# Kernel optimization log

Hardware: AMD Instinct MI355X
Metric: run time of the kernel (lower is better)

The kernel has to match this reference:

```python
import jax, jax.numpy as jnp
import numpy as np

B, K, V = 8192, 1024, 2


def setup_inputs() -> dict:
    key = jax.random.key(0)
    k1, k2, k3, k4, k5, k6 = jax.random.split(key, 6)
    z = jax.random.normal(k1, (B, K), dtype=jnp.float32)
    # -1 means no intervention for that sample
    intervention_target = jax.random.randint(k2, (B,), -1, K)
    intervention_variant = jax.random.randint(k3, (B,), 0, V)
    raw_adjacency = jax.random.normal(k4, (K, K), dtype=jnp.float32) * 0.05
    intervention_means = jax.random.normal(k5, (K, V), dtype=jnp.float32)
    intervention_log_scales = jax.random.normal(k6, (K, V), dtype=jnp.float32) * 0.1
    return {
        "z": z,
        "intervention_target": intervention_target,
        "intervention_variant": intervention_variant,
        "raw_adjacency": raw_adjacency,
        "intervention_means": intervention_means,
        "intervention_log_scales": intervention_log_scales,
    }


def _scm_forward(z, target, variant, raw_adjacency, means, log_scales):
    Kd = z.shape[1]
    # strictly-lower-triangular adjacency (row j holds parents of node j)
    A = raw_adjacency * jnp.tril(jnp.ones((Kd, Kd), z.dtype), k=-1)

    def step(u, xs):
        a_row, mean_row, logsc_row, z_j, j = xs
        # forward substitution: u_j = z_j + sum_{i<j} A[j,i] * u_i
        # columns >= j of u are still zero and A row is zero there too
        value = z_j + u @ a_row  # [B]
        # intervention overwrite for samples with target == j
        m = mean_row[variant]                 # [B]
        s = jnp.exp(logsc_row[variant])       # [B]
        value = jnp.where(target == j, m + s * z_j, value)
        u = jax.lax.dynamic_update_slice(u, value[:, None], (0, j))
        return u, None

    u0 = jnp.zeros_like(z)
    xs = (A, means, log_scales, z.T, jnp.arange(Kd))
    u, _ = jax.lax.scan(step, u0, xs)
    return u


def reference(z, intervention_target, intervention_variant, raw_adjacency,
              intervention_means, intervention_log_scales):
    return _scm_forward(z, intervention_target, intervention_variant,
                        raw_adjacency, intervention_means, intervention_log_scales)
```

## Files before the change

### kernel.cpp

```cpp
#include <hip/hip_runtime.h>
#include <hip/hip_bf16.h>
#include <cstdint>

#define KDIM 1024
#define BDIM 8192
#define VDIM 2
#define NBLK 16

#if defined(__has_builtin)
#if __has_builtin(__builtin_amdgcn_global_load_lds)
#define HAS_GLL 1
#endif
#endif
#ifndef HAS_GLL
#define HAS_GLL 0
#endif

typedef __attribute__((ext_vector_type(8))) short short8;
typedef __attribute__((ext_vector_type(4))) float f32x4;

__device__ inline unsigned short f2bf(float x) {
  unsigned u = __builtin_bit_cast(unsigned, x);
  u = (u + 0x7FFFu + ((u >> 16) & 1u)) >> 16;
  return (unsigned short)u;
}

__device__ inline float bf2f(unsigned short x) {
  return __builtin_bit_cast(float, (unsigned)x << 16);
}

__device__ inline void qtile_map(int t, int& bi, int& bj) {
  if (t < 64) {
    bi = t >> 3;
    bj = 8 + (t & 7);
  } else {
    int r = t - 64;
    const int c = r >> 4;
    r &= 15;
    bi = 8 * c + (r >> 2);
    bj = 8 * c + 4 + (r & 3);
  }
}


#define STAGE_T(DST, SRC, ROW0, COL0, LD)                                   \
  {                                                                         \
    const float* _s = (SRC);                                                \
    _Pragma("unroll") for (int _p = 0; _p < 4; ++_p) {                      \
      const int _m = _p * 16 + rw;                                          \
      float4 _v = *(const float4*)(_s + (size_t)((ROW0) + _m) * (LD) +      \
                                   (COL0) + 4 * k4);                        \
      (DST)[4 * k4 + 0][_m] = _v.x;                                         \
      (DST)[4 * k4 + 1][_m] = _v.y;                                         \
      (DST)[4 * k4 + 2][_m] = _v.z;                                         \
      (DST)[4 * k4 + 3][_m] = _v.w;                                         \
    }                                                                       \
  }

#define STAGE_D(DST, SRC, ROW0, COL0, LD)                                   \
  {                                                                         \
    const float* _s = (SRC);                                                \
    _Pragma("unroll") for (int _p = 0; _p < 4; ++_p) {                      \
      const int _kk = _p * 16 + rw;                                         \
      *(float4*)&(DST)[_kk][4 * k4] =                                       \
          *(const float4*)(_s + (size_t)((ROW0) + _kk) * (LD) + (COL0) +    \
                           4 * k4);                                         \
    }                                                                       \
  }

#define ZERO_ACC                                                            \
  _Pragma("unroll") for (int _a = 0; _a < 4; ++_a)                          \
      _Pragma("unroll") for (int _b = 0; _b < 4; ++_b) acc[_a][_b] = 0.f;

__device__ __forceinline__ void mac64(const float (*Ls)[68],
                                      const float (*Rs)[68], int tm, int tn,
                                      float acc[4][4]) {
#pragma unroll 4
  for (int k = 0; k < 64; ++k) {
    const float4 av = *(const float4*)&Ls[k][4 * tm];
    const float4 bv = *(const float4*)&Rs[k][4 * tn];
    const float aa[4] = {av.x, av.y, av.z, av.w};
    const float bb4[4] = {bv.x, bv.y, bv.z, bv.w};
#pragma unroll
    for (int a = 0; a < 4; ++a)
#pragma unroll
      for (int b = 0; b < 4; ++b) acc[a][b] += aa[a] * bb4[b];
  }
}

#define STORE_MT(R0, C0)                                                    \
  _Pragma("unroll") for (int _a = 0; _a < 4; ++_a) {                        \
    *(float4*)(MT + (size_t)((R0) + 4 * tm + _a) * KDIM + (C0) + 4 * tn) =  \
        make_float4(acc[_a][0], acc[_a][1], acc[_a][2], acc[_a][3]);        \
  }

#define MBF_TILE(R0, C0, BUF)                                               \
  {                                                                         \
    __syncthreads();                                                        \
    _Pragma("unroll") for (int _a = 0; _a < 4; ++_a)                        \
        _Pragma("unroll") for (int _b = 0; _b < 4; ++_b)                    \
            (BUF)[4 * tm + _a][4 * tn + _b] = acc[_a][_b];                  \
    __syncthreads();                                                        \
    const int _tr = tid >> 4, _tc = tid & 15;                               \
    _Pragma("unroll") for (int _p = 0; _p < 4; ++_p) {                      \
      const int _il = _p * 16 + _tr;                                        \
      ushort4 _o;                                                           \
      _o.x = f2bf((BUF)[4 * _tc + 0][_il]);                                 \
      _o.y = f2bf((BUF)[4 * _tc + 1][_il]);                                 \
      _o.z = f2bf((BUF)[4 * _tc + 2][_il]);                                 \
      _o.w = f2bf((BUF)[4 * _tc + 3][_il]);                                 \
      *(ushort4*)(Mbf + (size_t)((C0) + _il) * KDIM + (R0) + 4 * _tc) = _o; \
    }                                                                       \
  }

__global__ __launch_bounds__(256) void comb01(const float* __restrict__ A,
                                              float* __restrict__ MT,
                                              unsigned short* __restrict__ Mbf,
                                              const float* __restrict__ Z,
                                              unsigned short* __restrict__ Zbf,
                                              float* __restrict__ Pscr,
                                              int do_zbf) {
  if (blockIdx.x >= NBLK) {
    const int wid = blockIdx.x - NBLK;
    const int nw = gridDim.x - NBLK;
    const int idx0 = wid * 256 + threadIdx.x;
    const int stride = nw * 256;
    const float4 z4 = make_float4(0.f, 0.f, 0.f, 0.f);
    const uint4 u4 = make_uint4(0u, 0u, 0u, 0u);

    for (int i = idx0; i < 256 * 1024; i += stride) {
      const int blk = i >> 10, off = i & 1023;
      const int bi = blk >> 4, bj = blk & 15;
      if (bi <= bj) continue;
      *(float4*)(MT + (size_t)(bi * 64 + (off >> 4)) * KDIM + bj * 64 +
                 4 * (off & 15)) = z4;
    }
    for (int i = idx0; i < 96 * 1024; i += stride) {
      const int t = i >> 10, off = i & 1023;
      int bi, bj;
      qtile_map(t, bi, bj);
      *(float4*)(MT + (size_t)(bi * 64 + (off >> 4)) * KDIM + bj * 64 +
                 4 * (off & 15)) = z4;
    }
    for (int i = idx0; i < 98304; i += stride)
      *(float4*)(Pscr + 4 * (size_t)i) = z4;
    for (int i = idx0; i < 256 * 512; i += stride) {
      const int blk = i >> 9, off = i & 511;
      const int bi = blk >> 4, bj = blk & 15;
      if (bi >= bj) continue;
      *(uint4*)(Mbf + (size_t)(bi * 64 + (off >> 3)) * KDIM + bj * 64 +
                8 * (off & 7)) = u4;
    }
    if (do_zbf) {
      for (int i = idx0; i < BDIM * KDIM / 4; i += stride) {
        float4 v = *(const float4*)(Z + 4 * (size_t)i);
        ushort4 o;
        o.x = f2bf(v.x);
        o.y = f2bf(v.y);
        o.z = f2bf(v.z);
        o.w = f2bf(v.w);
        *(ushort4*)(Zbf + 4 * (size_t)i) = o;
      }
    }
    return;
  }

  int b = blockIdx.x;
  const int rt = b & 1;
  const int jt = (b >> 1) & 1;
  const int s = b >> 2;
  const int base = s * 256;

  __shared__ float shpool[6 * 64 * 68];
  float (*Ls)[68] = (float(*)[68])(shpool);
  float (*Rs)[68] = (float(*)[68])(shpool + 4352);
  float (*tQ0L)[68] = (float(*)[68])(shpool + 2 * 4352);
  float (*tQ0H)[68] = (float(*)[68])(shpool + 3 * 4352);
  float (*tP0)[68] = (float(*)[68])(shpool + 4 * 4352);
  float (*tP1)[68] = (float(*)[68])(shpool + 5 * 4352);

  const int tid = threadIdx.x;
  const int k4 = tid & 15;
  const int rw = tid >> 4;
  const int tm = tid >> 4;
  const int tn = tid & 15;
  float acc[4][4];

  {
    float* Tt = shpool;
    float* As4 = shpool + 2 * 4352;
    const int g = tid >> 6;
    const int l = tid & 63;
    const int dbase = base + g * 64;
    float* Asg = As4 + g * 4160;

    for (int r = 0; r < 64; ++r)
      Asg[r * 65 + l] = A[(size_t)(dbase + r) * KDIM + dbase + l];
    __syncthreads();

    {
      const int h = l >> 5, c = l & 31;
      const float* Ah = Asg + (32 * h) * 65 + 32 * h;
      float m[32];
#pragma unroll
      for (int r = 0; r < 32; ++r) m[r] = (r == c) ? 1.f : 0.f;
#pragma unroll
      for (int r = 1; r < 32; ++r) {
        float a0 = 0.f, a1 = 0.f;
#pragma unroll
        for (int i = 0; i < 32; ++i) {
          if (i >= r) break;
          if (i & 1) a1 += Ah[r * 65 + i] * m[i];
          else       a0 += Ah[r * 65 + i] * m[i];
        }
        const float v = a0 + a1;
        m[r] = (r > c) ? v : m[r];
      }
      float* Th = Tt + g * 2112 + h * 1056;
#pragma unroll
      for (int r = 0; r < 32; ++r) Th[r * 33 + c] = m[r];
    }
    __syncthreads();

    const int tm8 = l >> 3, tn8 = l & 7;
    {
      float u[4][4];
#pragma unroll
      for (int a = 0; a < 4; ++a)
#pragma unroll
        for (int b2 = 0; b2 < 4; ++b2) u[a][b2] = 0.f;
      const float* T1 = Tt + g * 2112;
#pragma unroll
      for (int ki = 0; ki < 8; ++ki) {
        float4 av[4], bv[4];
#pragma unroll
        for (int a = 0; a < 4; ++a)
          av[a] = *(const float4*)&Asg[(32 + 4 * tm8 + a) * 65 + 4 * ki];
#pragma unroll
        for (int j = 0; j < 4; ++j)
          bv[j] = *(const float4*)&T1[(4 * ki + j) * 33 + 4 * tn8];
#pragma unroll
        for (int a = 0; a < 4; ++a) {
          const float aa[4] = {av[a].x, av[a].y, av[a].z, av[a].w};
#pragma unroll
          for (int j = 0; j < 4; ++j) {
            const float bb[4] = {bv[j].x, bv[j].y, bv[j].z, bv[j].w};
#pragma unroll
            for (int b2 = 0; b2 < 4; ++b2) u[a][b2] += aa[j] * bb[b2];
          }
        }
      }
#pragma unroll
      for (int a = 0; a < 4; ++a)
#pragma unroll
        for (int b2 = 0; b2 < 4; ++b2)
          Asg[(4 * tm8 + a) * 32 + 4 * tn8 + b2] = u[a][b2];
    }
    __syncthreads();

    {
      float t21[4][4];
#pragma unroll
      for (int a = 0; a < 4; ++a)
#pragma unroll
        for (int b2 = 0; b2 < 4; ++b2) t21[a][b2] = 0.f;
      const float* T2 = Tt + g * 2112 + 1056;
#pragma unroll
      for (int ki = 0; ki < 8; ++ki) {
        float4 av[4], bv[4];
#pragma unroll
        for (int a = 0; a < 4; ++a)
          av[a] = *(const float4*)&T2[(4 * tm8 + a) * 33 + 4 * ki];
#pragma unroll
        for (int j = 0; j < 4; ++j)
          bv[j] = *(const float4*)&Asg[(4 * ki + j) * 32 + 4 * tn8];
#pragma unroll
        for (int a = 0; a < 4; ++a) {
          const float aa[4] = {av[a].x, av[a].y, av[a].z, av[a].w};
#pragma unroll
          for (int j = 0; j < 4; ++j) {
            const float bb[4] = {bv[j].x, bv[j].y, bv[j].z, bv[j].w};
#pragma unroll
            for (int b2 = 0; b2 < 4; ++b2) t21[a][b2] += aa[j] * bb[b2];
          }
        }
      }
#pragma unroll
      for (int a = 0; a < 4; ++a)
#pragma unroll
        for (int b2 = 0; b2 < 4; ++b2)
          Asg[1024 + (4 * tm8 + a) * 32 + 4 * tn8 + b2] = t21[a][b2];
    }
    __syncthreads();

    {
      const float* T21 = Asg + 1024;
      const float* Tg = Tt + g * 2112;
      for (int r4 = 0; r4 < 16; ++r4) {
        float vals[4];
#pragma unroll
        for (int j = 0; j < 4; ++j) {
          const int r = 4 * r4 + j;
          float v;
          if (r < 32)
            v = (l < 32) ? Tg[r * 33 + l] : 0.f;
          else
            v = (l < 32) ? T21[(r - 32) * 32 + l]
                         : Tg[1056 + (r - 32) * 33 + (l - 32)];
          vals[j] = v;
        }
        *(float4*)(MT + (size_t)(dbase + l) * KDIM + dbase + 4 * r4) =
            make_float4(vals[0], vals[1], vals[2], vals[3]);
      }
      if (jt == 0 && rt == 0) {
        for (int r = 0; r < 64; ++r) {
          float v;
          if (r < 32)
            v = (l < 32) ? Tg[r * 33 + l] : 0.f;
          else
            v = (l < 32) ? T21[(r - 32) * 32 + l]
                         : Tg[1056 + (r - 32) * 33 + (l - 32)];
          Mbf[(size_t)(dbase + r) * KDIM + dbase + l] = f2bf(v);
        }
      }
    }
    __syncthreads();
  }

  if (jt == 0) {
    STAGE_T(Ls, MT, base, base, KDIM);
    STAGE_T(Rs, A, base + 64, base, KDIM);
    __syncthreads();
    ZERO_ACC;
    mac64(Ls, Rs, tm, tn, acc);
    __syncthreads();
#pragma unroll
    for (int a = 0; a < 4; ++a)
#pragma unroll
      for (int b2 = 0; b2 < 4; ++b2) tP0[4 * tn + b2][4 * tm + a] = acc[a][b2];
    STAGE_D(Rs, MT, base + 64, base + 64, KDIM);
    __syncthreads();
    ZERO_ACC;
    mac64(tP0, Rs, tm, tn, acc);
    __syncthreads();
#pragma unroll
    for (int a = 0; a < 4; ++a)
#pragma unroll
      for (int b2 = 0; b2 < 4; ++b2) tQ0L[4 * tn + b2][4 * tm + a] = acc[a][b2];
    if (rt == 0) {
      STORE_MT(base, base + 64);
      MBF_TILE(base, base + 64, Rs);
    }
  }
  __syncthreads();

  if (rt == 1) {
    STAGE_T(Ls, MT, base + 128, base + 128, KDIM);
    STAGE_T(Rs, A, base + 192, base + 128, KDIM);
    __syncthreads();
    ZERO_ACC;
    mac64(Ls, Rs, tm, tn, acc);
    __syncthreads();
#pragma unroll
    for (int a = 0; a < 4; ++a)
#pragma unroll
      for (int b2 = 0; b2 < 4; ++b2) tP1[4 * tn + b2][4 * tm + a] = acc[a][b2];
    STAGE_D(Rs, MT, base + 192, base + 192, KDIM);
    __syncthreads();
    ZERO_ACC;
    mac64(tP1, Rs, tm, tn, acc);
    __syncthreads();
#pragma unroll
    for (int a = 0; a < 4; ++a)
#pragma unroll
      for (int b2 = 0; b2 < 4; ++b2) tQ0H[4 * tm + a][4 * tn + b2] = acc[a][b2];
    if (jt == 1) {
      STORE_MT(base + 128, base + 192);
      MBF_TILE(base + 128, base + 192, Rs);
    }
  }
  __syncthreads();

  STAGE_T(Ls, MT, base + 64 * jt, base + 64 * jt, KDIM);
  __syncthreads();
  for (int kb2 = 0; kb2 <= rt; ++kb2) {
    ZERO_ACC;
    for (int kb = jt; kb < 2; ++kb) {
      STAGE_T(Rs, A, base + 128 + 64 * kb2, base + 64 * kb, KDIM);
      __syncthreads();
      mac64(kb == jt ? Ls : tQ0L, Rs, tm, tn, acc);
      __syncthreads();
    }
    if (kb2 == 0) {
#pragma unroll
      for (int a = 0; a < 4; ++a)
#pragma unroll
        for (int b2 = 0; b2 < 4; ++b2) tP0[4 * tn + b2][4 * tm + a] = acc[a][b2];
    } else {
#pragma unroll
      for (int a = 0; a < 4; ++a)
#pragma unroll
        for (int b2 = 0; b2 < 4; ++b2) tP1[4 * tn + b2][4 * tm + a] = acc[a][b2];
    }
  }
  __syncthreads();

  ZERO_ACC;
  if (rt == 0) {
    STAGE_D(Rs, MT, base + 128, base + 128, KDIM);
    __syncthreads();
    mac64(tP0, Rs, tm, tn, acc);
    __syncthreads();
  } else {
    mac64(tP0, tQ0H, tm, tn, acc);
    __syncthreads();
    STAGE_D(Rs, MT, base + 192, base + 192, KDIM);
    __syncthreads();
    mac64(tP1, Rs, tm, tn, acc);
    __syncthreads();
  }
  STORE_MT(base + 64 * jt, base + 128 + 64 * rt);
  MBF_TILE(base + 64 * jt, base + 128 + 64 * rt, Rs);
}

template <int T>
__global__ __launch_bounds__(256) void comb_p(const float* __restrict__ A,
                                              const float* __restrict__ MT,
                                              float* __restrict__ Pt) {
  int b = blockIdx.x;
  const int kc = b % T; b /= T;
  const int rt = b % T; b /= T;
  const int jt = b % T; b /= T;
  const int c = b;
  if (kc < jt) return;
  const int h = 64 * T;
  const int base = c * 2 * h;

  __shared__ float Ls[64][68];
  __shared__ float Rs[64][68];
  const int tid = threadIdx.x;
  const int k4 = tid & 15;
  const int rw = tid >> 4;
  const int tm = tid >> 4;
  const int tn = tid & 15;
  float acc[4][4];
  ZERO_ACC;

  STAGE_T(Ls, MT, base + 64 * jt, base + 64 * kc, KDIM);
  STAGE_T(Rs, A, base + h + 64 * rt, base + 64 * kc, KDIM);
  __syncthreads();
  mac64(Ls, Rs, tm, tn, acc);

  float* P0 = Pt + (size_t)c * h * h;
#pragma unroll
  for (int a = 0; a < 4; ++a)
#pragma unroll
    for (int b2 = 0; b2 < 4; ++b2)
      unsafeAtomicAdd(P0 + (size_t)(64 * jt + 4 * tm + a) * h + 64 * rt +
                          4 * tn + b2,
                      acc[a][b2]);
}

template <int T>
__global__ __launch_bounds__(256) void comb_q(float* __restrict__ MT,
                                              const float* __restrict__ Pt) {
  int b = blockIdx.x;
  const int kc = b % T; b /= T;
  const int rt = b % T; b /= T;
  const int jt = b % T; b /= T;
  const int c = b;
  if (kc > rt) return;
  const int h = 64 * T;
  const int base = c * 2 * h;

  __shared__ float Ls[64][68];
  __shared__ float Rs[64][68];
  const int tid = threadIdx.x;
  const int k4 = tid & 15;
  const int rw = tid >> 4;
  const int tm = tid >> 4;
  const int tn = tid & 15;
  float acc[4][4];
  ZERO_ACC;

  const float* P0 = Pt + (size_t)c * h * h;
  STAGE_T(Ls, P0, 64 * jt, 64 * kc, h);
  STAGE_D(Rs, MT, base + h + 64 * kc, base + h + 64 * rt, KDIM);
  __syncthreads();
  mac64(Ls, Rs, tm, tn, acc);

#pragma unroll
  for (int a = 0; a < 4; ++a)
#pragma unroll
    for (int b2 = 0; b2 < 4; ++b2)
      unsafeAtomicAdd(MT + (size_t)(base + 64 * jt + 4 * tm + a) * KDIM +
                          base + h + 64 * rt + 4 * tn + b2,
                      acc[a][b2]);
}

__global__ __launch_bounds__(256) void mt2bf96(const float* __restrict__ MT,
                                               unsigned short* __restrict__ Mbf) {
  int bi, bj;
  qtile_map(blockIdx.x, bi, bj);
  const int j0 = bi * 64;
  const int i0 = bj * 64;
  __shared__ float tile[64][65];

  const int tr = threadIdx.x >> 4;
  const int tc = threadIdx.x & 15;
#pragma unroll
  for (int p = 0; p < 4; ++p) {
    const int rj = p * 16 + tr;
    float4 v = *(const float4*)(MT + (size_t)(j0 + rj) * KDIM + i0 + 4 * tc);
    tile[rj][4 * tc + 0] = v.x;
    tile[rj][4 * tc + 1] = v.y;
    tile[rj][4 * tc + 2] = v.z;
    tile[rj][4 * tc + 3] = v.w;
  }
  __syncthreads();
#pragma unroll
  for (int p = 0; p < 4; ++p) {
    const int il = p * 16 + tr;
    ushort4 o;
    o.x = f2bf(tile[4 * tc + 0][il]);
    o.y = f2bf(tile[4 * tc + 1][il]);
    o.z = f2bf(tile[4 * tc + 2][il]);
    o.w = f2bf(tile[4 * tc + 3][il]);
    *(ushort4*)(Mbf + (size_t)(i0 + il) * KDIM + j0 + 4 * tc) = o;
  }
}

#define LDB 72

template <int ZBF>
__global__ __launch_bounds__(256) void gemm_mfma(
    const float* __restrict__ Z, const unsigned short* __restrict__ Zbf,
    const unsigned short* __restrict__ Mbf, const float* __restrict__ MT,
    const int* __restrict__ tgt, const int* __restrict__ var,
    const float* __restrict__ means, const float* __restrict__ lsc,
    float* __restrict__ C) {
  __shared__ unsigned short As[128][LDB];
#if HAS_GLL
  __shared__ unsigned short Bs[128][64];
#else
  __shared__ unsigned short Bs[128][LDB];
#endif
  __shared__ float scoef[128];
  __shared__ int stb[128];

  const int d = blockIdx.x;
  const int xbl = d & 7;
  const int nir = (d >> 3) & 7;
  const int xbh = d >> 6;
  const int xb = xbh * 8 + xbl;
  const int ni = (xb & 32) ? (7 - nir) : nir;
  const int b0 = xb * 128;
  const int i0 = ni * 128;

  const int tid = threadIdx.x;
  const int w = tid >> 6;
  const int lane = tid & 63;
  const int wr = w >> 1, wc = w & 1;
  const int mlane = lane & 15;
  const int q = lane >> 4;

  const int rq = tid >> 4, kq = tid & 15;
  const int cb = tid >> 3, ck = tid & 7;

  f32x4 acc[4][4];
#pragma unroll
  for (int a = 0; a < 4; ++a)
#pragma unroll
    for (int b = 0; b < 4; ++b) acc[a][b] = (f32x4){0.f, 0.f, 0.f, 0.f};

  const int nkb = 2 * (ni + 1);
  for (int kb = 0; kb < nkb; ++kb) {
    const int k0 = kb * 64;
    if (ZBF) {
#pragma unroll
      for (int p = 0; p < 4; ++p) {
        const int r = p * 32 + cb;
        *(uint4*)&As[r][8 * ck] =
            *(const uint4*)(Zbf + (size_t)(b0 + r) * KDIM + k0 + 8 * ck);
      }
    } else {
#pragma unroll
      for (int p = 0; p < 8; ++p) {
        const int r = p * 16 + rq;
        float4 zv = *(const float4*)(Z + (size_t)(b0 + r) * KDIM + k0 + 4 * kq);
        ushort4 o;
        o.x = f2bf(zv.x);
        o.y = f2bf(zv.y);
        o.z = f2bf(zv.z);
        o.w = f2bf(zv.w);
        *(ushort4*)&As[r][4 * kq] = o;
      }
    }
#if HAS_GLL
    {
      const int rl = lane >> 3;
      const int ch = lane & 7;
#pragma unroll
      for (int i = 0; i < 4; ++i) {
        const int row = w * 32 + i * 8 + rl;
        const int sch = ch ^ (row & 7);
        const unsigned short* src =
            Mbf + (size_t)(i0 + row) * KDIM + k0 + sch * 8;
        __builtin_amdgcn_global_load_lds(
            (const __attribute__((address_space(1))) void*)src,
            (__attribute__((address_space(3))) void*)&Bs[w * 32 + i * 8][0],
            16, 0, 0);
      }
    }
#else
#pragma unroll
    for (int p = 0; p < 4; ++p) {
      const int c = p * 32 + cb;
      *(uint4*)&Bs[c][8 * ck] =
          *(const uint4*)(Mbf + (size_t)(i0 + c) * KDIM + k0 + 8 * ck);
    }
#endif
    __syncthreads();
#pragma unroll
    for (int ks = 0; ks < 2; ++ks) {
      const int kf = ks * 32 + q * 8;
      short8 av[4], bv[4];
#pragma unroll
      for (int a = 0; a < 4; ++a)
        av[a] = *(const short8*)&As[wr * 64 + 16 * a + mlane][kf];
#if HAS_GLL
      const char* BsB = (const char*)&Bs[0][0];
#pragma unroll
      for (int b = 0; b < 4; ++b) {
        const int row = wc * 64 + 16 * b + mlane;
        bv[b] = *(const short8*)(BsB + row * 128 +
                                 ((2 * kf) ^ ((row & 7) << 4)));
      }
#else
#pragma unroll
      for (int b = 0; b < 4; ++b)
        bv[b] = *(const short8*)&Bs[wc * 64 + 16 * b + mlane][kf];
#endif
#pragma unroll
      for (int a = 0; a < 4; ++a)
#pragma unroll
        for (int b = 0; b < 4; ++b)
          acc[a][b] =
              __builtin_amdgcn_mfma_f32_16x16x32_bf16(av[a], bv[b], acc[a][b], 0, 0, 0);
    }
    __syncthreads();
  }

  {
    const int s = tid >> 1, h2 = tid & 1;
    const int br = b0 + s;
    const int tb = tgt[br];
    float part = 0.f;
    if (tb >= 0) {
      const int nk16 = (tb >> 4) + 1;
      if (ZBF) {
        const unsigned short* zr = Zbf + (size_t)br * KDIM;
        const unsigned short* mr = Mbf + (size_t)tb * KDIM;
        for (int c16 = h2; c16 < nk16; c16 += 2) {
          const uint4 za = *(const uint4*)(zr + c16 * 16);
          const uint4 zb2 = *(const uint4*)(zr + c16 * 16 + 8);
          const uint4 ma = *(const uint4*)(mr + c16 * 16);
          const uint4 mb2 = *(const uint4*)(mr + c16 * 16 + 8);
          const unsigned zw[8] = {za.x, za.y, za.z, za.w,
                                  zb2.x, zb2.y, zb2.z, zb2.w};
          const unsigned mw[8] = {ma.x, ma.y, ma.z, ma.w,
                                  mb2.x, mb2.y, mb2.z, mb2.w};
#pragma unroll
          for (int wv = 0; wv < 8; ++wv) {
            part += __builtin_bit_cast(float, zw[wv] << 16) *
                    __builtin_bit_cast(float, mw[wv] << 16);
            part += __builtin_bit_cast(float, zw[wv] & 0xFFFF0000u) *
                    __builtin_bit_cast(float, mw[wv] & 0xFFFF0000u);
          }
        }
      } else {
        const float* zr = Z + (size_t)br * KDIM;
        const unsigned short* mr = Mbf + (size_t)tb * KDIM;
        const int nk8 = (tb >> 3) + 1;
        for (int c8 = h2; c8 < nk8; c8 += 2) {
          const float4 z0 = *(const float4*)(zr + c8 * 8);
          const float4 z1 = *(const float4*)(zr + c8 * 8 + 4);
          const ushort4 m0 = *(const ushort4*)(mr + c8 * 8);
          const ushort4 m1 = *(const ushort4*)(mr + c8 * 8 + 4);
          part += z0.x * bf2f(m0.x) + z0.y * bf2f(m0.y) + z0.z * bf2f(m0.z) +
                  z0.w * bf2f(m0.w) + z1.x * bf2f(m1.x) + z1.y * bf2f(m1.y) +
                  z1.z * bf2f(m1.z) + z1.w * bf2f(m1.w);
        }
      }
    }
    part += __shfl_down(part, 1);
    if (h2 == 0) {
      float cf = 0.f;
      int tbs = 0;
      if (tb >= 0) {
        const int v = var[br];
        const float mval = means[tb * VDIM + v];
        const float sval = expf(lsc[tb * VDIM + v]);
        const float zv = Z[(size_t)br * KDIM + tb];
        cf = (mval + sval * zv) - part;
        tbs = tb;
      }
      scoef[s] = cf;
      stb[s] = tbs;
    }
  }
  __syncthreads();

#pragma unroll
  for (int a = 0; a < 4; ++a) {
    const int l0 = wr * 64 + 16 * a + q * 4;
    const int row0 = b0 + l0;
#pragma unroll
    for (int b = 0; b < 4; ++b) {
      const int col = i0 + wc * 64 + 16 * b + mlane;
      float* Cp = C + (size_t)row0 * KDIM + col;
#pragma unroll
      for (int j = 0; j < 4; ++j) {
        const float cf = scoef[l0 + j];
        const float corr = cf * MT[(size_t)stb[l0 + j] * KDIM + col];
        Cp[j * KDIM] = acc[a][b][j] + corr;
      }
    }
  }
}

extern "C" void kernel_launch(void* const* d_in, const int* in_sizes, int n_in,
                              void* d_out, int out_size, void* d_ws,
                              size_t ws_size, hipStream_t stream) {
  const float* z = (const float*)d_in[0];
  const int* tgt = (const int*)d_in[1];
  const int* var = (const int*)d_in[2];
  const float* A = (const float*)d_in[3];
  const float* means = (const float*)d_in[4];
  const float* lsc = (const float*)d_in[5];
  float* out = (float*)d_out;

  char* ws = (char*)d_ws;
  float* MT = (float*)ws;
  unsigned short* Mbf = (unsigned short*)(ws + (4u << 20));
  float* Pt2 = (float*)(ws + (6u << 20));
  float* Pt3 = (float*)(ws + (6u << 20) + (512u << 10));
  unsigned short* Zbf = (unsigned short*)(ws + (7u << 20) + (512u << 10));
  const int use_zbf =
      ws_size >= (7u << 20) + (512u << 10) + (size_t)BDIM * KDIM * 2 ? 1 : 0;

  hipLaunchKernelGGL(comb01, dim3(256), dim3(256), 0, stream, A, MT, Mbf, z,
                     Zbf, Pt2, use_zbf);
  hipLaunchKernelGGL((comb_p<4>), dim3(128), dim3(256), 0, stream, A, MT, Pt2);
  hipLaunchKernelGGL((comb_q<4>), dim3(128), dim3(256), 0, stream, MT, Pt2);
  hipLaunchKernelGGL((comb_p<8>), dim3(512), dim3(256), 0, stream, A, MT, Pt3);
  hipLaunchKernelGGL((comb_q<8>), dim3(512), dim3(256), 0, stream, MT, Pt3);
  hipLaunchKernelGGL(mt2bf96, dim3(96), dim3(256), 0, stream, MT, Mbf);
  if (use_zbf)
    hipLaunchKernelGGL((gemm_mfma<1>), dim3((BDIM / 128) * (KDIM / 128)),
                       dim3(256), 0, stream, z, Zbf, Mbf, MT, tgt, var, means,
                       lsc, out);
  else
    hipLaunchKernelGGL((gemm_mfma<0>), dim3((BDIM / 128) * (KDIM / 128)),
                       dim3(256), 0, stream, z, Zbf, Mbf, MT, tgt, var, means,
                       lsc, out);
}
```

Baseline: 228.7 us.

## Split the fused 256-wide inverse stage into a 128-wide stage plus extra combine level

The first kernel used to invert 256x256 diagonal blocks with 16 blocks doing multi-step combines. It now inverts only 128x128 blocks, using 8 blocks in which only half the threads do the 64x64 triangular inverses. A new comb_p<2>/comb_q<2> launch pair then combines those into 256-wide blocks, and the zeroing and bf16 conversion ranges grow to cover the extra off-diagonal tiles. This shortens the serial chain inside the first kernel, at the cost of two more launches, idle threads in that kernel, and atomic-add based combining.

```diff
diff --git a/kernel.cpp b/kernel.cpp
--- a/kernel.cpp
+++ b/kernel.cpp
@@ -33,12 +33,18 @@
   if (t < 64) {
     bi = t >> 3;
     bj = 8 + (t & 7);
-  } else {
+  } else if (t < 96) {
     int r = t - 64;
     const int c = r >> 4;
     r &= 15;
     bi = 8 * c + (r >> 2);
     bj = 8 * c + 4 + (r & 3);
+  } else {
+    int r = t - 96;
+    const int c = r >> 2;
+    r &= 3;
+    bi = 4 * c + (r >> 1);
+    bj = 4 * c + 2 + (r & 1);
   }
 }
 
@@ -113,16 +119,16 @@
     }                                                                       \
   }
 
-__global__ __launch_bounds__(256) void comb01(const float* __restrict__ A,
+__global__ __launch_bounds__(256) void comb0a(const float* __restrict__ A,
                                               float* __restrict__ MT,
                                               unsigned short* __restrict__ Mbf,
                                               const float* __restrict__ Z,
                                               unsigned short* __restrict__ Zbf,
                                               float* __restrict__ Pscr,
                                               int do_zbf) {
-  if (blockIdx.x >= NBLK) {
-    const int wid = blockIdx.x - NBLK;
-    const int nw = gridDim.x - NBLK;
+  if (blockIdx.x >= 8) {
+    const int wid = blockIdx.x - 8;
+    const int nw = gridDim.x - 8;
     const int idx0 = wid * 256 + threadIdx.x;
     const int stride = nw * 256;
     const float4 z4 = make_float4(0.f, 0.f, 0.f, 0.f);
@@ -135,14 +141,14 @@
       *(float4*)(MT + (size_t)(bi * 64 + (off >> 4)) * KDIM + bj * 64 +
                  4 * (off & 15)) = z4;
     }
-    for (int i = idx0; i < 96 * 1024; i += stride) {
+    for (int i = idx0; i < 112 * 1024; i += stride) {
       const int t = i >> 10, off = i & 1023;
       int bi, bj;
       qtile_map(t, bi, bj);
       *(float4*)(MT + (size_t)(bi * 64 + (off >> 4)) * KDIM + bj * 64 +
                  4 * (off & 15)) = z4;
     }
-    for (int i = idx0; i < 98304; i += stride)
+    for (int i = idx0; i < 114688; i += stride)
       *(float4*)(Pscr + 4 * (size_t)i) = z4;
     for (int i = idx0; i < 256 * 512; i += stride) {
       const int blk = i >> 9, off = i & 511;
@@ -165,19 +171,13 @@
     return;
   }
 
-  int b = blockIdx.x;
-  const int rt = b & 1;
-  const int jt = (b >> 1) & 1;
-  const int s = b >> 2;
-  const int base = s * 256;
-
-  __shared__ float shpool[6 * 64 * 68];
-  float (*Ls)[68] = (float(*)[68])(shpool);
-  float (*Rs)[68] = (float(*)[68])(shpool + 4352);
-  float (*tQ0L)[68] = (float(*)[68])(shpool + 2 * 4352);
-  float (*tQ0H)[68] = (float(*)[68])(shpool + 3 * 4352);
-  float (*tP0)[68] = (float(*)[68])(shpool + 4 * 4352);
-  float (*tP1)[68] = (float(*)[68])(shpool + 5 * 4352);
+  const int p = blockIdx.x;
+  const int pb = p * 128;
+
+  __shared__ float pool[3 * 4352];
+  float (*Ls)[68] = (float(*)[68])(pool);
+  float (*Rs)[68] = (float(*)[68])(pool + 4352);
+  float (*tP0)[68] = (float(*)[68])(pool + 2 * 4352);
 
   const int tid = threadIdx.x;
   const int k4 = tid & 15;
@@ -187,18 +187,20 @@
   float acc[4][4];
 
   {
-    float* Tt = shpool;
-    float* As4 = shpool + 2 * 4352;
+    float* Tt = pool;
+    float* As2 = pool + 4352;
     const int g = tid >> 6;
     const int l = tid & 63;
-    const int dbase = base + g * 64;
-    float* Asg = As4 + g * 4160;
-
-    for (int r = 0; r < 64; ++r)
-      Asg[r * 65 + l] = A[(size_t)(dbase + r) * KDIM + dbase + l];
+    const int dbase = pb + g * 64;
+    float* Asg = As2 + g * 4160;
+
+    if (g < 2) {
+      for (int r = 0; r < 64; ++r)
+        Asg[r * 65 + l] = A[(size_t)(dbase + r) * KDIM + dbase + l];
+    }
     __syncthreads();
 
-    {
+    if (g < 2) {
       const int h = l >> 5, c = l & 31;
       const float* Ah = Asg + (32 * h) * 65 + 32 * h;
       float m[32];
@@ -222,8 +224,8 @@
     }
     __syncthreads();
 
-    const int tm8 = l >> 3, tn8 = l & 7;
-    {
+    const int tm8 = (tid & 63) >> 3, tn8 = tid & 7;
+    if (g < 2) {
       float u[4][4];
 #pragma unroll
       for (int a = 0; a < 4; ++a)
@@ -258,7 +260,7 @@
     }
     __syncthreads();
 
-    {
+    if (g < 2) {
       float t21[4][4];
 #pragma unroll
       for (int a = 0; a < 4; ++a)
@@ -293,7 +295,7 @@
     }
     __syncthreads();
 
-    {
+    if (g < 2) {
       const float* T21 = Asg + 1024;
       const float* Tg = Tt + g * 2112;
       for (int r4 = 0; r4 < 16; ++r4) {
@@ -312,115 +314,35 @@
         *(float4*)(MT + (size_t)(dbase + l) * KDIM + dbase + 4 * r4) =
             make_float4(vals[0], vals[1], vals[2], vals[3]);
       }
-      if (jt == 0 && rt == 0) {
-        for (int r = 0; r < 64; ++r) {
-          float v;
-          if (r < 32)
-            v = (l < 32) ? Tg[r * 33 + l] : 0.f;
-          else
-            v = (l < 32) ? T21[(r - 32) * 32 + l]
-                         : Tg[1056 + (r - 32) * 33 + (l - 32)];
-          Mbf[(size_t)(dbase + r) * KDIM + dbase + l] = f2bf(v);
-        }
+      for (int r = 0; r < 64; ++r) {
+        float v;
+        if (r < 32)
+          v = (l < 32) ? Tg[r * 33 + l] : 0.f;
+        else
+          v = (l < 32) ? T21[(r - 32) * 32 + l]
+                       : Tg[1056 + (r - 32) * 33 + (l - 32)];
+        Mbf[(size_t)(dbase + r) * KDIM + dbase + l] = f2bf(v);
       }
     }
     __syncthreads();
   }
 
-  if (jt == 0) {
-    STAGE_T(Ls, MT, base, base, KDIM);
-    STAGE_T(Rs, A, base + 64, base, KDIM);
-    __syncthreads();
-    ZERO_ACC;
-    mac64(Ls, Rs, tm, tn, acc);
-    __syncthreads();
-#pragma unroll
-    for (int a = 0; a < 4; ++a)
-#pragma unroll
-      for (int b2 = 0; b2 < 4; ++b2) tP0[4 * tn + b2][4 * tm + a] = acc[a][b2];
-    STAGE_D(Rs, MT, base + 64, base + 64, KDIM);
-    __syncthreads();
-    ZERO_ACC;
-    mac64(tP0, Rs, tm, tn, acc);
-    __syncthreads();
-#pragma unroll
-    for (int a = 0; a < 4; ++a)
-#pragma unroll
-      for (int b2 = 0; b2 < 4; ++b2) tQ0L[4 * tn + b2][4 * tm + a] = acc[a][b2];
-    if (rt == 0) {
-      STORE_MT(base, base + 64);
-      MBF_TILE(base, base + 64, Rs);
-    }
-  }
+  STAGE_T(Ls, MT, pb, pb, KDIM);
+  STAGE_T(Rs, A, pb + 64, pb, KDIM);
   __syncthreads();
-
-  if (rt == 1) {
-    STAGE_T(Ls, MT, base + 128, base + 128, KDIM);
-    STAGE_T(Rs, A, base + 192, base + 128, KDIM);
-    __syncthreads();
-    ZERO_ACC;
-    mac64(Ls, Rs, tm, tn, acc);
-    __syncthreads();
-#pragma unroll
-    for (int a = 0; a < 4; ++a)
-#pragma unroll
-      for (int b2 = 0; b2 < 4; ++b2) tP1[4 * tn + b2][4 * tm + a] = acc[a][b2];
-    STAGE_D(Rs, MT, base + 192, base + 192, KDIM);
-    __syncthreads();
-    ZERO_ACC;
-    mac64(tP1, Rs, tm, tn, acc);
-    __syncthreads();
-#pragma unroll
-    for (int a = 0; a < 4; ++a)
-#pragma unroll
-      for (int b2 = 0; b2 < 4; ++b2) tQ0H[4 * tm + a][4 * tn + b2] = acc[a][b2];
-    if (jt == 1) {
-      STORE_MT(base + 128, base + 192);
-      MBF_TILE(base + 128, base + 192, Rs);
-    }
-  }
+  ZERO_ACC;
+  mac64(Ls, Rs, tm, tn, acc);
   __syncthreads();
-
-  STAGE_T(Ls, MT, base + 64 * jt, base + 64 * jt, KDIM);
+#pragma unroll
+  for (int a = 0; a < 4; ++a)
+#pragma unroll
+    for (int b2 = 0; b2 < 4; ++b2) tP0[4 * tn + b2][4 * tm + a] = acc[a][b2];
+  STAGE_D(Rs, MT, pb + 64, pb + 64, KDIM);
   __syncthreads();
-  for (int kb2 = 0; kb2 <= rt; ++kb2) {
-    ZERO_ACC;
-    for (int kb = jt; kb < 2; ++kb) {
-      STAGE_T(Rs, A, base + 128 + 64 * kb2, base + 64 * kb, KDIM);
-      __syncthreads();
-      mac64(kb == jt ? Ls : tQ0L, Rs, tm, tn, acc);
-      __syncthreads();
-    }
-    if (kb2 == 0) {
-#pragma unroll
-      for (int a = 0; a < 4; ++a)
-#pragma unroll
-        for (int b2 = 0; b2 < 4; ++b2) tP0[4 * tn + b2][4 * tm + a] = acc[a][b2];
-    } else {
-#pragma unroll
-      for (int a = 0; a < 4; ++a)
-#pragma unroll
-        for (int b2 = 0; b2 < 4; ++b2) tP1[4 * tn + b2][4 * tm + a] = acc[a][b2];
-    }
-  }
-  __syncthreads();
-
   ZERO_ACC;
-  if (rt == 0) {
-    STAGE_D(Rs, MT, base + 128, base + 128, KDIM);
-    __syncthreads();
-    mac64(tP0, Rs, tm, tn, acc);
-    __syncthreads();
-  } else {
-    mac64(tP0, tQ0H, tm, tn, acc);
-    __syncthreads();
-    STAGE_D(Rs, MT, base + 192, base + 192, KDIM);
-    __syncthreads();
-    mac64(tP1, Rs, tm, tn, acc);
-    __syncthreads();
-  }
-  STORE_MT(base + 64 * jt, base + 128 + 64 * rt);
-  MBF_TILE(base + 64 * jt, base + 128 + 64 * rt, Rs);
+  mac64(tP0, Rs, tm, tn, acc);
+  STORE_MT(pb, pb + 64);
+  MBF_TILE(pb, pb + 64, Rs);
 }
 
 template <int T>
@@ -498,8 +420,8 @@
                       acc[a][b2]);
 }
 
-__global__ __launch_bounds__(256) void mt2bf96(const float* __restrict__ MT,
-                                               unsigned short* __restrict__ Mbf) {
+__global__ __launch_bounds__(256) void mt2bf112(const float* __restrict__ MT,
+                                                unsigned short* __restrict__ Mbf) {
   int bi, bj;
   qtile_map(blockIdx.x, bi, bj);
   const int j0 = bi * 64;
@@ -743,19 +665,22 @@
   char* ws = (char*)d_ws;
   float* MT = (float*)ws;
   unsigned short* Mbf = (unsigned short*)(ws + (4u << 20));
-  float* Pt2 = (float*)(ws + (6u << 20));
-  float* Pt3 = (float*)(ws + (6u << 20) + (512u << 10));
-  unsigned short* Zbf = (unsigned short*)(ws + (7u << 20) + (512u << 10));
+  float* Pt1 = (float*)(ws + (6u << 20));
+  float* Pt2 = (float*)(ws + (6u << 20) + (256u << 10));
+  float* Pt3 = (float*)(ws + (6u << 20) + (768u << 10));
+  unsigned short* Zbf = (unsigned short*)(ws + (7u << 20) + (768u << 10));
   const int use_zbf =
-      ws_size >= (7u << 20) + (512u << 10) + (size_t)BDIM * KDIM * 2 ? 1 : 0;
-
-  hipLaunchKernelGGL(comb01, dim3(256), dim3(256), 0, stream, A, MT, Mbf, z,
-                     Zbf, Pt2, use_zbf);
+      ws_size >= (7u << 20) + (768u << 10) + (size_t)BDIM * KDIM * 2 ? 1 : 0;
+
+  hipLaunchKernelGGL(comb0a, dim3(256), dim3(256), 0, stream, A, MT, Mbf, z,
+                     Zbf, Pt1, use_zbf);
+  hipLaunchKernelGGL((comb_p<2>), dim3(32), dim3(256), 0, stream, A, MT, Pt1);
+  hipLaunchKernelGGL((comb_q<2>), dim3(32), dim3(256), 0, stream, MT, Pt1);
   hipLaunchKernelGGL((comb_p<4>), dim3(128), dim3(256), 0, stream, A, MT, Pt2);
   hipLaunchKernelGGL((comb_q<4>), dim3(128), dim3(256), 0, stream, MT, Pt2);
   hipLaunchKernelGGL((comb_p<8>), dim3(512), dim3(256), 0, stream, A, MT, Pt3);
   hipLaunchKernelGGL((comb_q<8>), dim3(512), dim3(256), 0, stream, MT, Pt3);
-  hipLaunchKernelGGL(mt2bf96, dim3(96), dim3(256), 0, stream, MT, Mbf);
+  hipLaunchKernelGGL(mt2bf112, dim3(112), dim3(256), 0, stream, MT, Mbf);
   if (use_zbf)
     hipLaunchKernelGGL((gemm_mfma<1>), dim3((BDIM / 128) * (KDIM / 128)),
                        dim3(256), 0, stream, z, Zbf, Mbf, MT, tgt, var, means,
```

Result: faster. 213.9 us (-6.5%).
